# Performance work log

Hardware: AMD Instinct MI355X
Metric: run time of the kernel (lower is better)

The kernel has to match this reference:

```python
import jax, jax.numpy as jnp
import numpy as np

TAPS = 5
DELAY = 3
EPS_POWER = 1e-7   # clamp for inverse power (wpe_one_iteration eps)
EPS_REG = 1e-10    # diagonal loading of the correlation matrix


def setup_inputs() -> dict:
    key = jax.random.key(0)
    ks = jax.random.split(key, 5)
    B, F, C, T = 8, 257, 8, 800
    shp = (B, F, C, T)
    return {
        "data_sep_real": jax.random.normal(ks[0], shp, jnp.float32),
        "data_sep_imag": jax.random.normal(ks[1], shp, jnp.float32),
        "data_mix_real": jax.random.normal(ks[2], shp, jnp.float32),
        "data_mix_imag": jax.random.normal(ks[3], shp, jnp.float32),
        "ilens": jax.random.randint(ks[4], (B,), 1, T + 1, jnp.int32),
    }


def _ytilde(Y, taps, delay):
    # Y: (B,F,C,T) complex -> stacked delayed taps (B,F,taps*C,T)
    # tap k at time t holds Y[..., t - delay - k] (zero-padded past)
    B, F, C, T = Y.shape
    Yp = jnp.pad(Y, ((0, 0), (0, 0), (0, 0), (delay + taps - 1, 0)))
    tilde = jnp.stack(
        [Yp[..., taps - 1 - k: taps - 1 - k + T] for k in range(taps)], axis=2
    )  # (B,F,taps,C,T)
    return tilde.reshape(B, F, taps * C, T)


def _wpe_one_iteration(Y, power, taps, delay):
    # Y: (B,F,C,T) complex, power: (B,F,T) real
    B, F, C, T = Y.shape
    inv_power = 1.0 / jnp.maximum(power, EPS_POWER)          # (B,F,T)
    Yt = _ytilde(Y, taps, delay)                              # (B,F,K,T), K=taps*C
    t0 = delay + taps - 1                                     # correlations use t >= t0
    Ytv = Yt[..., t0:]
    Yv = Y[..., t0:]
    Ytw = Ytv * inv_power[:, :, None, t0:].astype(Y.dtype)
    # R = sum_t w(t) Ytilde(t) Ytilde(t)^H  -> (B,F,K,K)
    R = jnp.einsum('bfat,bfct->bfac', Ytw, jnp.conj(Ytv))
    # P = sum_t w(t) Ytilde(t) Y(t)^H      -> (B,F,K,C)
    P = jnp.einsum('bfat,bfet->bfae', Ytw, jnp.conj(Yv))
    K = taps * C
    R = R + EPS_REG * jnp.eye(K, dtype=R.dtype)
    G = jnp.linalg.solve(R, P)                                # (B,F,K,C)
    # X(t) = Y(t) - G^H Ytilde(t)
    X = Y - jnp.einsum('bfae,bfat->bfet', jnp.conj(G), Yt)
    return X


def reference(data_sep_real, data_sep_imag, data_mix_real, data_mix_imag, ilens):
    # power of separated signal, averaged over channels (use_dnn_mask=False)
    power = jnp.mean(data_sep_real ** 2 + data_sep_imag ** 2, axis=-2)  # (B,F,T)
    Ym = jax.lax.complex(data_mix_real, data_mix_imag)                  # (B,F,C,T)
    X = _wpe_one_iteration(Ym, power, TAPS, DELAY)
    # zero out padded frames: t >= ilens[b]
    t = jnp.arange(X.shape[-1])
    valid = t[None, :] < ilens[:, None]                                 # (B,T)
    X = jnp.where(valid[:, None, None, :], X, 0)
    # return real/imag stacked on last axis: (B,F,C,T,2)
    return jnp.stack([X.real, X.imag], axis=-1)
```

## Files before the change

kernel.cpp:

```cpp
#include <hip/hip_runtime.h>

#define B 8
#define F 257
#define C 8
#define T 800
#define TAPS 5
#define DELAY 3
#define K 40
#define NCOL 48
#define T0 7
#define BF (B*F)

typedef __bf16 bf16x8 __attribute__((ext_vector_type(8)));
typedef __bf16 bf16x4 __attribute__((ext_vector_type(4)));
typedef float f32x4 __attribute__((ext_vector_type(4)));

struct PF { float4 v[3]; };

__device__ __forceinline__ void dma16(const void* g, void* l) {
    __builtin_amdgcn_global_load_lds(
        (const __attribute__((address_space(1))) void*)g,
        (__attribute__((address_space(3))) void*)l, 16, 0, 0);
}

__global__ __launch_bounds__(256) void power_kernel(const float* __restrict__ sr,
                                                    const float* __restrict__ si,
                                                    float* __restrict__ W) {
    int bf = blockIdx.x;
    const float* srp = sr + (size_t)bf * C * T;
    const float* sip = si + (size_t)bf * C * T;
    int t0 = threadIdx.x * 4;
    if (t0 < T) {
        float s[4] = {0.f, 0.f, 0.f, 0.f};
#pragma unroll
        for (int c = 0; c < C; ++c) {
            float4 a = *(const float4*)(srp + c * T + t0);
            float4 b = *(const float4*)(sip + c * T + t0);
            s[0] = fmaf(a.x, a.x, fmaf(b.x, b.x, s[0]));
            s[1] = fmaf(a.y, a.y, fmaf(b.y, b.y, s[1]));
            s[2] = fmaf(a.z, a.z, fmaf(b.z, b.z, s[2]));
            s[3] = fmaf(a.w, a.w, fmaf(b.w, b.w, s[3]));
        }
        float4 w;
        float* wp = (float*)&w;
#pragma unroll
        for (int e = 0; e < 4; ++e) {
            float v = fmaxf(s[e] * (1.0f / C), 1e-7f);
            wp[e] = (t0 + e < T0) ? 0.f : rsqrtf(v);
        }
        *(float4*)(W + (size_t)bf * T + t0) = w;
    }
}

#define WB2 12800

__global__ __launch_bounds__(256, 3) void rp_mfma_kernel(const float* __restrict__ mr,
                                                         const float* __restrict__ mi,
                                                         const float* __restrict__ W,
                                                         float2* __restrict__ Rout,
                                                         float2* __restrict__ Pout) {
    __shared__ __align__(16) unsigned char SH[4 * WB2];
    const int lane = threadIdx.x & 63;
    const int wid = threadIdx.x >> 6;
    const int bf = blockIdx.x * 4 + wid;
    unsigned char* base = SH + wid * WB2;
    unsigned char* b0 = base + 7680;
    unsigned char* b1 = base + 10240;

    const float* mrp = mr + (size_t)bf * C * T;
    const float* mip = mi + (size_t)bf * C * T;
    const float* Wp  = W  + (size_t)bf * T;

    const int q = lane >> 4, col = lane & 15;
    const int pc = lane >> 3, pg = lane & 7;

    const int PM[6] = {0, 0, 0, 1, 1, 2};
    const int PN[6] = {0, 1, 2, 1, 2, 2};

    const float* sdma[2]; const float* sdma0[2]; bool haldma[2];
#pragma unroll
    for (int it = 0; it < 2; ++it) {
        int task = lane + it * 64;
        int row = task / 10, grp = task - row * 10;
        int pl = row >> 3, c = row & 7;
        const float* cb = (pl ? mip : mrp) + c * T;
        sdma[it] = cb + grp * 4 - 8;
        haldma[it] = (grp < 2);
        sdma0[it] = haldma[it] ? cb : sdma[it];
    }
    const bool tact = lane < 32;
    {
    }
    int ttask = 128 + (tact ? lane : 0);
    int trow = ttask / 10, tgrp = ttask - trow * 10;
    int tpl = trow >> 3, tc = trow & 7;
    const float* tcb = (tpl ? mip : mrp) + tc * T;
    const float* tsrc = tcb + tgrp * 4 - 8;
    const bool thal = (tgrp < 2);
    const float* tsrc0 = thal ? tcb : tsrc;
    const float* wsrc = Wp + pg * 4;

    f32x4 accRe[6], accIr[6], accRi[6];
#pragma unroll
    for (int p = 0; p < 6; ++p) {
        accRe[p] = (f32x4){0.f, 0.f, 0.f, 0.f};
        accIr[p] = (f32x4){0.f, 0.f, 0.f, 0.f};
        accRi[p] = (f32x4){0.f, 0.f, 0.f, 0.f};
    }

    dma16(sdma0[0], b0 + lane * 16);
    dma16(sdma0[1], b0 + 1024 + lane * 16);
    float4 ty = tact ? *(const float4*)tsrc0 : make_float4(0.f, 0.f, 0.f, 0.f);
    float4 wcur = *(const float4*)wsrc;
    asm volatile("s_waitcnt vmcnt(0)" ::: "memory");
#pragma unroll
    for (int it = 0; it < 2; ++it)
        if (haldma[it])
            *(float4*)(b0 + it * 1024 + lane * 16) = make_float4(0.f, 0.f, 0.f, 0.f);
    if (thal) ty = make_float4(0.f, 0.f, 0.f, 0.f);
    __builtin_amdgcn_sched_barrier(0);

    for (int ks = 0; ks < 25; ++ks) {
        unsigned char* buf = (ks & 1) ? b1 : b0;
        unsigned char* nbuf = (ks & 1) ? b0 : b1;
        if (tact) *(float4*)(buf + 2048 + lane * 16) = ty;
        if (ks < 24) {
            int ntb = (ks + 1) * 32;
            dma16(sdma[0] + ntb, nbuf + lane * 16);
            dma16(sdma[1] + ntb, nbuf + 1024 + lane * 16);
        }
        asm volatile("s_waitcnt vmcnt(2)" ::: "memory");
        __builtin_amdgcn_sched_barrier(0);

        {
            const float* yrr = (const float*)(buf + pc * 160);
            const float* yir = (const float*)(buf + (8 + pc) * 160);
            float yre[12], yim[12];
            float4 r0 = *(const float4*)(yrr + pg * 4);
            float4 r1 = *(const float4*)(yrr + pg * 4 + 4);
            float4 r2 = *(const float4*)(yrr + pg * 4 + 8);
            float4 i0 = *(const float4*)(yir + pg * 4);
            float4 i1 = *(const float4*)(yir + pg * 4 + 4);
            float4 i2 = *(const float4*)(yir + pg * 4 + 8);
            yre[0] = r0.x; yre[1] = r0.y; yre[2]  = r0.z; yre[3]  = r0.w;
            yre[4] = r1.x; yre[5] = r1.y; yre[6]  = r1.z; yre[7]  = r1.w;
            yre[8] = r2.x; yre[9] = r2.y; yre[10] = r2.z; yre[11] = r2.w;
            yim[0] = i0.x; yim[1] = i0.y; yim[2]  = i0.z; yim[3]  = i0.w;
            yim[4] = i1.x; yim[5] = i1.y; yim[6]  = i1.z; yim[7]  = i1.w;
            yim[8] = i2.x; yim[9] = i2.y; yim[10] = i2.z; yim[11] = i2.w;
            float wv[4] = {wcur.x, wcur.y, wcur.z, wcur.w};
#pragma unroll
            for (int v = 0; v < 6; ++v) {
                int row = (v < 5) ? (v * 8 + pc) : (40 + pc);
                int off = (v < 5) ? (5 - v) : 8;
                bf16x4 zr, zi;
#pragma unroll
                for (int e = 0; e < 4; ++e) {
                    zr[e] = (__bf16)(wv[e] * yre[off + e]);
                    zi[e] = (__bf16)(wv[e] * yim[off + e]);
                }
                *(bf16x4*)(base + row * 80 + pg * 8) = zr;
                *(bf16x4*)(base + 3840 + row * 80 + pg * 8) = zi;
            }
        }

        bf16x8 fr[3], fi[3];
#pragma unroll
        for (int X = 0; X < 3; ++X) {
            fr[X] = *(const bf16x8*)(base + (X * 16 + col) * 80 + q * 16);
            fi[X] = *(const bf16x8*)(base + 3840 + (X * 16 + col) * 80 + q * 16);
        }
#pragma unroll
        for (int p = 0; p < 6; ++p) {
            int mt = PM[p], nt = PN[p];
            accRe[p] = __builtin_amdgcn_mfma_f32_16x16x32_bf16(fr[mt], fr[nt], accRe[p], 0, 0, 0);
            accRe[p] = __builtin_amdgcn_mfma_f32_16x16x32_bf16(fi[mt], fi[nt], accRe[p], 0, 0, 0);
            accIr[p] = __builtin_amdgcn_mfma_f32_16x16x32_bf16(fi[mt], fr[nt], accIr[p], 0, 0, 0);
            accRi[p] = __builtin_amdgcn_mfma_f32_16x16x32_bf16(fr[mt], fi[nt], accRi[p], 0, 0, 0);
        }

        if (ks < 24) {
            int ntb = (ks + 1) * 32;
            if (tact) ty = *(const float4*)(tsrc + ntb);
            wcur = *(const float4*)(wsrc + ntb);
        }
    }

    float2* Rp = Rout + (size_t)bf * K * K;
    float2* Pp = Pout + (size_t)bf * K * C;
#pragma unroll
    for (int p = 0; p < 6; ++p) {
        int mt = PM[p], nt = PN[p];
#pragma unroll
        for (int r = 0; r < 4; ++r) {
            int m = mt * 16 + q * 4 + r;
            int n = nt * 16 + col;
            float re = accRe[p][r];
            float im = accIr[p][r] - accRi[p][r];
            if (m < K) {
                if (n < K) {
                    if (m == n) re += 1e-10f;
                    Rp[m * K + n] = make_float2(re, im);
                } else {
                    Pp[m * C + (n - K)] = make_float2(re, im);
                }
            }
            if (mt != nt && m < K && n < K)
                Rp[n * K + m] = make_float2(re, -im);
        }
    }
}

__device__ __forceinline__ float rdlane(float v, int j) {
    return __uint_as_float(__builtin_amdgcn_readlane(__float_as_uint(v), (unsigned)j));
}

__global__ __launch_bounds__(256) void solve_kernel(const float2* __restrict__ Rin,
                                                    const float2* __restrict__ Pin,
                                                    float2* __restrict__ Gout) {
    __shared__ float2 lbuf[2][64];
    const int bf = blockIdx.x;
    const int lane = threadIdx.x & 63;
    const int w = threadIdx.x >> 6;
    const bool act = lane < K;
    const int lr = act ? lane : 0;

    float2 colw[12];
    {
        const float2* Arow = Rin + (size_t)bf * K * K + (size_t)lr * K;
        const float2* Prow = Pin + (size_t)bf * K * C + (size_t)lr * C;
#pragma unroll
        for (int m = 0; m < 10; ++m) {
            float2 v = Arow[4 * m + w];
            colw[m] = act ? v : make_float2(0.f, 0.f);
        }
#pragma unroll
        for (int m = 10; m < 12; ++m) {
            float2 v = Prow[4 * (m - 10) + w];
            colw[m] = act ? v : make_float2(0.f, 0.f);
        }
    }

#pragma unroll
    for (int j = 0; j < K; ++j) {
        const int par = j & 1;
        const int wo = j & 3;
        const int mj = j >> 2;
        if (w == wo) {
            float dx = rdlane(colw[mj].x, j);
            float dy = rdlane(colw[mj].y, j);
            float den = fmaf(dx, dx, dy * dy);
            float r = 1.0f / den;
            float ix = dx * r, iy = -dy * r;
            float lx = colw[mj].x * ix - colw[mj].y * iy;
            float ly = colw[mj].x * iy + colw[mj].y * ix;
            bool isj = (lane == j);
            lx = isj ? (1.0f - ix) : lx;
            ly = isj ? (0.0f - iy) : ly;
            lbuf[par][lane] = make_float2(lx, ly);
        }
        __syncthreads();
        float2 l = lbuf[par][lane];
#pragma unroll
        for (int m = 0; m < 12; ++m) {
            if (4 * m + 3 <= j) continue;
            bool doit = (4 * m > j) || (4 * m + w > j);
            if (doit) {
                float ux = rdlane(colw[m].x, j);
                float uy = rdlane(colw[m].y, j);
                colw[m].x = fmaf(-l.x, ux, fmaf( l.y, uy, colw[m].x));
                colw[m].y = fmaf(-l.x, uy, fmaf(-l.y, ux, colw[m].y));
            }
        }
    }

    if (act) {
        float2* Gp = Gout + (size_t)bf * K * C + (size_t)lane * C;
        Gp[w]     = colw[10];
        Gp[4 + w] = colw[11];
    }
}

#define XSTR 144
#define XWB 12032

__device__ __forceinline__ PF x_load(const float* __restrict__ mrp,
                                     const float* __restrict__ mip,
                                     int tb, int lane) {
    PF p;
#pragma unroll
    for (int it = 0; it < 3; ++it) {
        int task = lane + it * 64;
        float4 v = make_float4(0.f, 0.f, 0.f, 0.f);
        if (task < 160) {
            int pl = task / 80;
            int rem = task - pl * 80;
            int c = rem / 10, grp = rem - c * 10;
            int tg = tb - 8 + grp * 4;
            const float* srcp = pl ? mip : mrp;
            if (tg >= 0) v = *(const float4*)(srcp + c * T + tg);
        }
        p.v[it] = v;
    }
    return p;
}

__device__ __forceinline__ void x_store(const PF& p, float* sre, float* sim_, int lane) {
#pragma unroll
    for (int it = 0; it < 3; ++it) {
        int task = lane + it * 64;
        if (task < 160) {
            int pl = task / 80;
            int rem = task - pl * 80;
            int c = rem / 10, grp = rem - c * 10;
            *(float4*)((pl ? sim_ : sre) + c * 44 + grp * 4) = p.v[it];
        }
    }
}

__global__ __launch_bounds__(64) void x_mfma_kernel(const float* __restrict__ mr,
                                                    const float* __restrict__ mi,
                                                    const float2* __restrict__ Gin,
                                                    const int* __restrict__ ilens,
                                                    float2* __restrict__ out) {
    __shared__ __align__(16) unsigned char SH[XWB];
    const int lane = threadIdx.x;
    const int gid = blockIdx.x;
    const int bf = gid >> 2;
    const int split = gid & 3;
    const int ck0 = (split == 0) ? 0 : (1 + split * 6);
    const int nck = (split == 0) ? 7 : 6;
    unsigned char* base = SH;
    float* sre = (float*)(base + 9216);
    float* sim_ = (float*)(base + 10624);

    const float* mrp = mr + (size_t)bf * C * T;
    const float* mip = mi + (size_t)bf * C * T;
    const float2* Gp = Gin + (size_t)bf * K * C;
    float2* outp = out + (size_t)bf * C * T;
    const int len = ilens[bf / F];

    const int q = lane >> 4, col = lane & 15;
    const int t2 = lane >> 1, half = lane & 1;

#pragma unroll
    for (int pl = 0; pl < 2; ++pl) {
        unsigned char* pb = base + pl * 4608 + t2 * XSTR + 80 + half * 24;
        *(float2*)(pb)      = make_float2(0.f, 0.f);
        *(float2*)(pb + 8)  = make_float2(0.f, 0.f);
        *(float2*)(pb + 16) = make_float2(0.f, 0.f);
    }

    bf16x8 Agr[2], Agi[2], Agin[2];
#pragma unroll
    for (int ks = 0; ks < 2; ++ks)
#pragma unroll
        for (int j = 0; j < 8; ++j) {
            int a = ks * 32 + q * 8 + j;
            float2 g = make_float2(0.f, 0.f);
            if (a < K && col < C) g = Gp[a * C + col];
            Agr[ks][j]  = (__bf16)g.x;
            Agi[ks][j]  = (__bf16)g.y;
            Agin[ks][j] = (__bf16)(-g.y);
        }

    PF cur = x_load(mrp, mip, ck0 * 32, lane);

    for (int ci = 0; ci < nck; ++ci) {
        const int tb = (ck0 + ci) * 32;

        x_store(cur, sre, sim_, lane);
        if (ci + 1 < nck) cur = x_load(mrp, mip, tb + 32, lane);

#pragma unroll
        for (int i = 0; i < 5; ++i) {
            int abase = half * 20 + 4 * i;
            bf16x4 zr, zi;
#pragma unroll
            for (int e2 = 0; e2 < 4; ++e2) {
                int a = abase + e2;
                int v = a >> 3, c = a & 7;
                int idx = c * 44 + t2 + 5 - v;
                zr[e2] = (__bf16)sre[idx];
                zi[e2] = (__bf16)sim_[idx];
            }
            *(bf16x4*)(base + t2 * XSTR + abase * 2) = zr;
            *(bf16x4*)(base + 4608 + t2 * XSTR + abase * 2) = zi;
        }

#pragma unroll
        for (int tt = 0; tt < 2; ++tt) {
            const int trow = tt * 16 + col;
            f32x4 accRe = (f32x4){0.f, 0.f, 0.f, 0.f};
            f32x4 accIm = (f32x4){0.f, 0.f, 0.f, 0.f};
#pragma unroll
            for (int ks = 0; ks < 2; ++ks) {
                bf16x8 byr = *(const bf16x8*)(base + trow * XSTR + ks * 64 + q * 16);
                bf16x8 byi = *(const bf16x8*)(base + 4608 + trow * XSTR + ks * 64 + q * 16);
                accRe = __builtin_amdgcn_mfma_f32_16x16x32_bf16(Agr[ks], byr, accRe, 0, 0, 0);
                accRe = __builtin_amdgcn_mfma_f32_16x16x32_bf16(Agi[ks], byi, accRe, 0, 0, 0);
                accIm = __builtin_amdgcn_mfma_f32_16x16x32_bf16(Agr[ks], byi, accIm, 0, 0, 0);
                accIm = __builtin_amdgcn_mfma_f32_16x16x32_bf16(Agin[ks], byr, accIm, 0, 0, 0);
            }
            if (q < 2) {
                int t = tb + tt * 16 + col;
                int l = tt * 16 + col + 8;
                bool ok = (t < len);
#pragma unroll
                for (int r = 0; r < 4; ++r) {
                    int e = q * 4 + r;
                    float yr = sre[e * 44 + l];
                    float yi = sim_[e * 44 + l];
                    float2 v = ok ? make_float2(yr - accRe[r], yi - accIm[r])
                                  : make_float2(0.f, 0.f);
                    outp[e * T + t] = v;
                }
            }
        }
    }
}

extern "C" void kernel_launch(void* const* d_in, const int* in_sizes, int n_in,
                              void* d_out, int out_size, void* d_ws, size_t ws_size,
                              hipStream_t stream) {
    const float* sep_r = (const float*)d_in[0];
    const float* sep_i = (const float*)d_in[1];
    const float* mix_r = (const float*)d_in[2];
    const float* mix_i = (const float*)d_in[3];
    const int* ilens   = (const int*)d_in[4];

    float* ws = (float*)d_ws;
    float* W = ws;
    float2* Rws = (float2*)(ws + (size_t)BF * T);
    float2* Gws = Rws + (size_t)BF * K * K;

    power_kernel<<<BF, 256, 0, stream>>>(sep_r, sep_i, W);
    rp_mfma_kernel<<<BF / 4, 256, 0, stream>>>(mix_r, mix_i, W, Rws, Gws);
    solve_kernel<<<BF, 256, 0, stream>>>(Rws, Gws, Gws);
    x_mfma_kernel<<<BF * 4, 64, 0, stream>>>(mix_r, mix_i, Gws, ilens, (float2*)d_out);
}
```

Measured before the change: 175.4 us.

## Replace LDS DMA staging of mixture data with direct register prefetch loads

Removes the global_load_lds double-buffered staging of the mixture signal and instead has each lane load its overlapping 12-sample window directly from global memory into registers, prefetching the next step before the MFMA block. This frees LDS (smaller per-wave footprint) and eliminates the extra LDS read and sync traffic. The cost is redundant global loads, since neighbouring lanes fetch overlapping windows, and higher register pressure from holding the prefetched values.

```diff
diff --git a/kernel.cpp b/kernel.cpp
--- a/kernel.cpp
+++ b/kernel.cpp
@@ -17,12 +17,6 @@
 
 struct PF { float4 v[3]; };
 
-__device__ __forceinline__ void dma16(const void* g, void* l) {
-    __builtin_amdgcn_global_load_lds(
-        (const __attribute__((address_space(1))) void*)g,
-        (__attribute__((address_space(3))) void*)l, 16, 0, 0);
-}
-
 __global__ __launch_bounds__(256) void power_kernel(const float* __restrict__ sr,
                                                     const float* __restrict__ si,
                                                     float* __restrict__ W) {
@@ -52,20 +46,18 @@
     }
 }
 
-#define WB2 12800
+#define WB3 7680
 
 __global__ __launch_bounds__(256, 3) void rp_mfma_kernel(const float* __restrict__ mr,
                                                          const float* __restrict__ mi,
                                                          const float* __restrict__ W,
                                                          float2* __restrict__ Rout,
                                                          float2* __restrict__ Pout) {
-    __shared__ __align__(16) unsigned char SH[4 * WB2];
+    __shared__ __align__(16) unsigned char SH[4 * WB3];
     const int lane = threadIdx.x & 63;
     const int wid = threadIdx.x >> 6;
     const int bf = blockIdx.x * 4 + wid;
-    unsigned char* base = SH + wid * WB2;
-    unsigned char* b0 = base + 7680;
-    unsigned char* b1 = base + 10240;
+    unsigned char* base = SH + wid * WB3;
 
     const float* mrp = mr + (size_t)bf * C * T;
     const float* mip = mi + (size_t)bf * C * T;
@@ -77,28 +69,9 @@
     const int PM[6] = {0, 0, 0, 1, 1, 2};
     const int PN[6] = {0, 1, 2, 1, 2, 2};
 
-    const float* sdma[2]; const float* sdma0[2]; bool haldma[2];
-#pragma unroll
-    for (int it = 0; it < 2; ++it) {
-        int task = lane + it * 64;
-        int row = task / 10, grp = task - row * 10;
-        int pl = row >> 3, c = row & 7;
-        const float* cb = (pl ? mip : mrp) + c * T;
-        sdma[it] = cb + grp * 4 - 8;
-        haldma[it] = (grp < 2);
-        sdma0[it] = haldma[it] ? cb : sdma[it];
-    }
-    const bool tact = lane < 32;
-    {
-    }
-    int ttask = 128 + (tact ? lane : 0);
-    int trow = ttask / 10, tgrp = ttask - trow * 10;
-    int tpl = trow >> 3, tc = trow & 7;
-    const float* tcb = (tpl ? mip : mrp) + tc * T;
-    const float* tsrc = tcb + tgrp * 4 - 8;
-    const bool thal = (tgrp < 2);
-    const float* tsrc0 = thal ? tcb : tsrc;
-    const float* wsrc = Wp + pg * 4;
+    const float* ysr = mrp + pc * T + pg * 4 - 8;
+    const float* ysi = mip + pc * T + pg * 4 - 8;
+    const float* wsr = Wp + pg * 4;
 
     f32x4 accRe[6], accIr[6], accRi[6];
 #pragma unroll
@@ -108,46 +81,31 @@
         accRi[p] = (f32x4){0.f, 0.f, 0.f, 0.f};
     }
 
-    dma16(sdma0[0], b0 + lane * 16);
-    dma16(sdma0[1], b0 + 1024 + lane * 16);
-    float4 ty = tact ? *(const float4*)tsrc0 : make_float4(0.f, 0.f, 0.f, 0.f);
-    float4 wcur = *(const float4*)wsrc;
-    asm volatile("s_waitcnt vmcnt(0)" ::: "memory");
-#pragma unroll
-    for (int it = 0; it < 2; ++it)
-        if (haldma[it])
-            *(float4*)(b0 + it * 1024 + lane * 16) = make_float4(0.f, 0.f, 0.f, 0.f);
-    if (thal) ty = make_float4(0.f, 0.f, 0.f, 0.f);
-    __builtin_amdgcn_sched_barrier(0);
+    float4 yr0, yr1, yr2, yi0, yi1, yi2, wcur;
+    {
+        const float* cbr = mrp + pc * T;
+        const float* cbi = mip + pc * T;
+        bool h0 = (pg < 2), h1 = (pg < 1);
+        yr0 = *(const float4*)(h0 ? cbr : ysr);
+        yr1 = *(const float4*)(h1 ? cbr : (ysr + 4));
+        yr2 = *(const float4*)(ysr + 8);
+        yi0 = *(const float4*)(h0 ? cbi : ysi);
+        yi1 = *(const float4*)(h1 ? cbi : (ysi + 4));
+        yi2 = *(const float4*)(ysi + 8);
+        wcur = *(const float4*)wsr;
+        if (h0) { yr0 = make_float4(0.f,0.f,0.f,0.f); yi0 = make_float4(0.f,0.f,0.f,0.f); }
+        if (h1) { yr1 = make_float4(0.f,0.f,0.f,0.f); yi1 = make_float4(0.f,0.f,0.f,0.f); }
+    }
 
     for (int ks = 0; ks < 25; ++ks) {
-        unsigned char* buf = (ks & 1) ? b1 : b0;
-        unsigned char* nbuf = (ks & 1) ? b0 : b1;
-        if (tact) *(float4*)(buf + 2048 + lane * 16) = ty;
-        if (ks < 24) {
-            int ntb = (ks + 1) * 32;
-            dma16(sdma[0] + ntb, nbuf + lane * 16);
-            dma16(sdma[1] + ntb, nbuf + 1024 + lane * 16);
-        }
-        asm volatile("s_waitcnt vmcnt(2)" ::: "memory");
-        __builtin_amdgcn_sched_barrier(0);
-
         {
-            const float* yrr = (const float*)(buf + pc * 160);
-            const float* yir = (const float*)(buf + (8 + pc) * 160);
             float yre[12], yim[12];
-            float4 r0 = *(const float4*)(yrr + pg * 4);
-            float4 r1 = *(const float4*)(yrr + pg * 4 + 4);
-            float4 r2 = *(const float4*)(yrr + pg * 4 + 8);
-            float4 i0 = *(const float4*)(yir + pg * 4);
-            float4 i1 = *(const float4*)(yir + pg * 4 + 4);
-            float4 i2 = *(const float4*)(yir + pg * 4 + 8);
-            yre[0] = r0.x; yre[1] = r0.y; yre[2]  = r0.z; yre[3]  = r0.w;
-            yre[4] = r1.x; yre[5] = r1.y; yre[6]  = r1.z; yre[7]  = r1.w;
-            yre[8] = r2.x; yre[9] = r2.y; yre[10] = r2.z; yre[11] = r2.w;
-            yim[0] = i0.x; yim[1] = i0.y; yim[2]  = i0.z; yim[3]  = i0.w;
-            yim[4] = i1.x; yim[5] = i1.y; yim[6]  = i1.z; yim[7]  = i1.w;
-            yim[8] = i2.x; yim[9] = i2.y; yim[10] = i2.z; yim[11] = i2.w;
+            yre[0] = yr0.x; yre[1] = yr0.y; yre[2]  = yr0.z; yre[3]  = yr0.w;
+            yre[4] = yr1.x; yre[5] = yr1.y; yre[6]  = yr1.z; yre[7]  = yr1.w;
+            yre[8] = yr2.x; yre[9] = yr2.y; yre[10] = yr2.z; yre[11] = yr2.w;
+            yim[0] = yi0.x; yim[1] = yi0.y; yim[2]  = yi0.z; yim[3]  = yi0.w;
+            yim[4] = yi1.x; yim[5] = yi1.y; yim[6]  = yi1.z; yim[7]  = yi1.w;
+            yim[8] = yi2.x; yim[9] = yi2.y; yim[10] = yi2.z; yim[11] = yi2.w;
             float wv[4] = {wcur.x, wcur.y, wcur.z, wcur.w};
 #pragma unroll
             for (int v = 0; v < 6; ++v) {
@@ -164,6 +122,18 @@
             }
         }
 
+        float4 nyr0, nyr1, nyr2, nyi0, nyi1, nyi2, nw;
+        if (ks < 24) {
+            int off = (ks + 1) * 32;
+            nyr0 = *(const float4*)(ysr + off);
+            nyr1 = *(const float4*)(ysr + off + 4);
+            nyr2 = *(const float4*)(ysr + off + 8);
+            nyi0 = *(const float4*)(ysi + off);
+            nyi1 = *(const float4*)(ysi + off + 4);
+            nyi2 = *(const float4*)(ysi + off + 8);
+            nw   = *(const float4*)(wsr + off);
+        }
+
         bf16x8 fr[3], fi[3];
 #pragma unroll
         for (int X = 0; X < 3; ++X) {
@@ -180,9 +150,9 @@
         }
 
         if (ks < 24) {
-            int ntb = (ks + 1) * 32;
-            if (tact) ty = *(const float4*)(tsrc + ntb);
-            wcur = *(const float4*)(wsrc + ntb);
+            yr0 = nyr0; yr1 = nyr1; yr2 = nyr2;
+            yi0 = nyi0; yi1 = nyi1; yi2 = nyi2;
+            wcur = nw;
         }
     }
 
```

After: 161.6 us. 7.9% less time.
